# Performance work log

Hardware: AMD Instinct MI355X
Metric: run time of the kernel (lower is better)

Reference implementation:

```python
import jax, jax.numpy as jnp
import numpy as np

N_NODES = 50000


def _gcn_norm(edge_index, num_nodes):
    # PyG GCNConv default: add self-loops, symmetric normalization D^-1/2 A D^-1/2
    src, dst = edge_index[0], edge_index[1]
    loops = jnp.arange(num_nodes, dtype=src.dtype)
    src = jnp.concatenate([src, loops])
    dst = jnp.concatenate([dst, loops])
    deg = jax.ops.segment_sum(jnp.ones_like(src, dtype=jnp.float32), dst,
                              num_segments=num_nodes)
    dis = jnp.where(deg > 0, jax.lax.rsqrt(jnp.maximum(deg, 1.0)), 0.0)
    norm = dis[src] * dis[dst]  # [E']
    return src, dst, norm


def _gcn_conv(x, W, b, src, dst, norm, num_nodes):
    h = x @ W                                   # [N, out] transform first
    msg = h[src] * norm[:, None]                # [E', out] gather + scale
    agg = jax.ops.segment_sum(msg, dst, num_segments=num_nodes)  # scatter-add
    return agg + b


def setup_inputs() -> dict:
    key = jax.random.key(0)
    k1, k2, k3, k4 = jax.random.split(key, 4)
    n, e, d_in, d_h = N_NODES, 800000, 256, 128
    basic_block = jax.random.normal(k1, (n, d_in), dtype=jnp.float32)
    edge_index = jax.random.randint(k2, (2, e), 0, n, dtype=jnp.int64)
    W1 = jax.random.normal(k3, (d_in, d_h), dtype=jnp.float32) * (1.0 / np.sqrt(d_in))
    b1 = jnp.zeros((d_h,), dtype=jnp.float32)
    W2 = jax.random.normal(k4, (d_h, d_h), dtype=jnp.float32) * (1.0 / np.sqrt(d_h))
    b2 = jnp.zeros((d_h,), dtype=jnp.float32)
    return {"basic_block": basic_block, "edge_index": edge_index,
            "W1": W1, "b1": b1, "W2": W2, "b2": b2}


def reference(basic_block, edge_index, W1, b1, W2, b2):
    n = basic_block.shape[0]
    src, dst, norm = _gcn_norm(edge_index, n)
    x = jax.nn.relu(_gcn_conv(basic_block, W1, b1, src, dst, norm, n))
    x = _gcn_conv(x, W2, b2, src, dst, norm, n)
    return x
```

## Files before the change

### kernel.cpp

```cpp
#include <hip/hip_runtime.h>
#include <hip/hip_bf16.h>
#include <stdint.h>

#define D_H 128

typedef __bf16 bf16_t;
typedef unsigned short u16;
typedef bf16_t bf16x8 __attribute__((ext_vector_type(8)));
typedef bf16_t bf16x4 __attribute__((ext_vector_type(4)));
typedef float  f32x4  __attribute__((ext_vector_type(4)));

__global__ void k_countrank(const int* __restrict__ dst, int* __restrict__ cnt,
                            u16* __restrict__ rank, int E, int crBlocks,
                            const float* __restrict__ W1, bf16_t* __restrict__ W1h,
                            bf16_t* __restrict__ W1l, int K1,
                            const float* __restrict__ W2, bf16_t* __restrict__ W2h,
                            bf16_t* __restrict__ W2l, int K2) {
    if ((int)blockIdx.x < crBlocks) {
        int e = blockIdx.x * 256 + threadIdx.x;
        if (e < E) rank[e] = (u16)atomicAdd(&cnt[dst[e]], 1);
        return;
    }
    int id = ((int)blockIdx.x - crBlocks) * 256 + threadIdx.x;
    int n1 = K1 * 128;
    if (id < n1) {
        int k = id >> 7, n = id & 127;
        float w = W1[id];
        bf16_t h = (bf16_t)w;
        W1h[(size_t)n * K1 + k] = h;
        W1l[(size_t)n * K1 + k] = (bf16_t)(w - (float)h);
    } else if (id < n1 + K2 * 128) {
        int id2 = id - n1;
        int k = id2 >> 7, n = id2 & 127;
        float w = W2[id2];
        bf16_t h = (bf16_t)w;
        W2h[(size_t)n * K2 + k] = h;
        W2l[(size_t)n * K2 + k] = (bf16_t)(w - (float)h);
    }
}

__global__ __launch_bounds__(1024) void k_scan1(const int* __restrict__ cnt,
                                                int* __restrict__ out,
                                                int* __restrict__ bsums,
                                                float* __restrict__ dis, int N) {
    __shared__ int tmp[1024];
    int t = threadIdx.x;
    int i = blockIdx.x * 1024 + t;
    int v = (i < N) ? cnt[i] : 0;
    if (i < N) dis[i] = 1.0f / sqrtf((float)(v + 1));
    tmp[t] = v;
    __syncthreads();
    for (int d = 1; d < 1024; d <<= 1) {
        int x = (t >= d) ? tmp[t - d] : 0;
        __syncthreads();
        tmp[t] += x;
        __syncthreads();
    }
    if (i < N) out[i] = tmp[t] - v;
    if (t == 1023) bsums[blockIdx.x] = tmp[t];
}

__global__ void k_scan2(int* __restrict__ bsums, int nb) {
    __shared__ int tmp[64];
    int t = threadIdx.x;
    int v = (t < nb) ? bsums[t] : 0;
    tmp[t] = v;
    __syncthreads();
    for (int d = 1; d < 64; d <<= 1) {
        int x = (t >= d) ? tmp[t - d] : 0;
        __syncthreads();
        tmp[t] += x;
        __syncthreads();
    }
    if (t < nb) bsums[t] = tmp[t] - v;
}

__global__ __launch_bounds__(1024) void k_scan3(int* __restrict__ off,
                                                const int* __restrict__ bsums,
                                                int N, int E) {
    int i = blockIdx.x * 1024 + threadIdx.x;
    if (i < N) off[i] += bsums[blockIdx.x];
    if (i == 0) off[N] = E;
}

#define LDK 40
#define FILL_PER 8
__global__ __launch_bounds__(128) void k_mm1fill(
        const float* __restrict__ Af,
        const bf16_t* __restrict__ Wh, const bf16_t* __restrict__ Wl,
        const float* __restrict__ dis, bf16_t* __restrict__ Cb,
        int N, int K,
        const int* __restrict__ src, const int* __restrict__ dst,
        const int* __restrict__ off, const u16* __restrict__ rank,
        u16* __restrict__ csr16, int E, int totThreads) {
    __shared__ bf16_t AsH[64][LDK];
    __shared__ bf16_t AsL[64][LDK];
    __shared__ bf16_t BsH[128][LDK];
    __shared__ bf16_t BsL[128][LDK];

    const int t    = threadIdx.x;
    const int lane = t & 63;
    const int wave = t >> 6;
    const int row0 = blockIdx.x * 64;
    const int wn   = wave * 64;
    const int fm   = lane & 15;
    const int fq   = lane >> 4;

    const int g = blockIdx.x * 128 + t;
    int epos[FILL_PER];
    u16 esrc[FILL_PER];
#pragma unroll
    for (int i = 0; i < FILL_PER; i++) {
        int e = g + i * totThreads;
        if (e < E) {
            int d = dst[e];
            epos[i] = off[d] + (int)rank[e];
            esrc[i] = (u16)src[e];
        } else {
            epos[i] = -1;
            esrc[i] = 0;
        }
    }

    f32x4 acc[4][4] = {};

    for (int k0 = 0; k0 < K; k0 += 32) {
        __syncthreads();
#pragma unroll
        for (int i = 0; i < 4; i++) {
            int idx = t + i * 128;
            int r   = idx >> 3;
            int c4  = idx & 7;
            int gr  = row0 + r;
            float4 v = make_float4(0.f, 0.f, 0.f, 0.f);
            if (gr < N) v = *(const float4*)(Af + (size_t)gr * K + k0 + c4 * 4);
            bf16_t h0 = (bf16_t)v.x, h1 = (bf16_t)v.y, h2 = (bf16_t)v.z, h3 = (bf16_t)v.w;
            bf16_t l0 = (bf16_t)(v.x - (float)h0);
            bf16_t l1 = (bf16_t)(v.y - (float)h1);
            bf16_t l2 = (bf16_t)(v.z - (float)h2);
            bf16_t l3 = (bf16_t)(v.w - (float)h3);
            *(bf16x4*)&AsH[r][c4 * 4] = (bf16x4){h0, h1, h2, h3};
            *(bf16x4*)&AsL[r][c4 * 4] = (bf16x4){l0, l1, l2, l3};
        }
#pragma unroll
        for (int i = 0; i < 4; i++) {
            int idx = t + i * 128;
            int r   = idx >> 2;
            int c8  = idx & 3;
            *(bf16x8*)&BsH[r][c8 * 8] = *(const bf16x8*)(Wh + (size_t)r * K + k0 + c8 * 8);
            *(bf16x8*)&BsL[r][c8 * 8] = *(const bf16x8*)(Wl + (size_t)r * K + k0 + c8 * 8);
        }
        __syncthreads();

        bf16x8 ah[4], al[4], bh[4], bl[4];
#pragma unroll
        for (int i = 0; i < 4; i++) {
            ah[i] = *(const bf16x8*)&AsH[i * 16 + fm][fq * 8];
            al[i] = *(const bf16x8*)&AsL[i * 16 + fm][fq * 8];
            bh[i] = *(const bf16x8*)&BsH[wn + i * 16 + fm][fq * 8];
            bl[i] = *(const bf16x8*)&BsL[wn + i * 16 + fm][fq * 8];
        }
#pragma unroll
        for (int mi = 0; mi < 4; mi++)
#pragma unroll
            for (int ni = 0; ni < 4; ni++) {
                acc[mi][ni] = __builtin_amdgcn_mfma_f32_16x16x32_bf16(ah[mi], bh[ni], acc[mi][ni], 0, 0, 0);
                acc[mi][ni] = __builtin_amdgcn_mfma_f32_16x16x32_bf16(ah[mi], bl[ni], acc[mi][ni], 0, 0, 0);
                acc[mi][ni] = __builtin_amdgcn_mfma_f32_16x16x32_bf16(al[mi], bh[ni], acc[mi][ni], 0, 0, 0);
            }
    }

#pragma unroll
    for (int mi = 0; mi < 4; mi++)
#pragma unroll
        for (int r = 0; r < 4; r++) {
            int grow = row0 + mi * 16 + fq * 4 + r;
            if (grow < N) {
                float dr = dis[grow];
#pragma unroll
                for (int ni = 0; ni < 4; ni++)
                    Cb[(size_t)grow * D_H + wn + ni * 16 + fm] = (bf16_t)(dr * acc[mi][ni][r]);
            }
        }

#pragma unroll
    for (int i = 0; i < FILL_PER; i++)
        if (epos[i] >= 0) csr16[epos[i]] = esrc[i];
}

__global__ __launch_bounds__(128) void k_mm2(const bf16_t* __restrict__ Ah,
                                             const bf16_t* __restrict__ Al,
                                             const bf16_t* __restrict__ Wh,
                                             const bf16_t* __restrict__ Wl,
                                             const float* __restrict__ dis,
                                             bf16_t* __restrict__ Cb,
                                             int N, int K) {
    __shared__ bf16_t AsH[64][LDK];
    __shared__ bf16_t AsL[64][LDK];
    __shared__ bf16_t BsH[128][LDK];
    __shared__ bf16_t BsL[128][LDK];

    const int t    = threadIdx.x;
    const int lane = t & 63;
    const int wave = t >> 6;
    const int row0 = blockIdx.x * 64;
    const int wn   = wave * 64;
    const int fm   = lane & 15;
    const int fq   = lane >> 4;

    f32x4 acc[4][4] = {};

    for (int k0 = 0; k0 < K; k0 += 32) {
        __syncthreads();
#pragma unroll
        for (int i = 0; i < 2; i++) {
            int idx = t + i * 128;
            int r   = idx >> 2;
            int c8  = idx & 3;
            int gr  = row0 + r;
            bf16x8 vh = {}, vl = {};
            if (gr < N) {
                vh = *(const bf16x8*)(Ah + (size_t)gr * K + k0 + c8 * 8);
                vl = *(const bf16x8*)(Al + (size_t)gr * K + k0 + c8 * 8);
            }
            *(bf16x8*)&AsH[r][c8 * 8] = vh;
            *(bf16x8*)&AsL[r][c8 * 8] = vl;
        }
#pragma unroll
        for (int i = 0; i < 4; i++) {
            int idx = t + i * 128;
            int r   = idx >> 2;
            int c8  = idx & 3;
            *(bf16x8*)&BsH[r][c8 * 8] = *(const bf16x8*)(Wh + (size_t)r * K + k0 + c8 * 8);
            *(bf16x8*)&BsL[r][c8 * 8] = *(const bf16x8*)(Wl + (size_t)r * K + k0 + c8 * 8);
        }
        __syncthreads();

        bf16x8 ah[4], al[4], bh[4], bl[4];
#pragma unroll
        for (int i = 0; i < 4; i++) {
            ah[i] = *(const bf16x8*)&AsH[i * 16 + fm][fq * 8];
            al[i] = *(const bf16x8*)&AsL[i * 16 + fm][fq * 8];
            bh[i] = *(const bf16x8*)&BsH[wn + i * 16 + fm][fq * 8];
            bl[i] = *(const bf16x8*)&BsL[wn + i * 16 + fm][fq * 8];
        }
#pragma unroll
        for (int mi = 0; mi < 4; mi++)
#pragma unroll
            for (int ni = 0; ni < 4; ni++) {
                acc[mi][ni] = __builtin_amdgcn_mfma_f32_16x16x32_bf16(ah[mi], bh[ni], acc[mi][ni], 0, 0, 0);
                acc[mi][ni] = __builtin_amdgcn_mfma_f32_16x16x32_bf16(ah[mi], bl[ni], acc[mi][ni], 0, 0, 0);
                acc[mi][ni] = __builtin_amdgcn_mfma_f32_16x16x32_bf16(al[mi], bh[ni], acc[mi][ni], 0, 0, 0);
            }
    }

#pragma unroll
    for (int mi = 0; mi < 4; mi++)
#pragma unroll
        for (int r = 0; r < 4; r++) {
            int grow = row0 + mi * 16 + fq * 4 + r;
            if (grow < N) {
                float dr = dis[grow];
#pragma unroll
                for (int ni = 0; ni < 4; ni++)
                    Cb[(size_t)grow * D_H + wn + ni * 16 + fm] = (bf16_t)(dr * acc[mi][ni][r]);
            }
        }
}

__global__ __launch_bounds__(256) void k_agg(const bf16_t* __restrict__ Hb,
                                             const float* __restrict__ dis,
                                             const int* __restrict__ off,
                                             const u16* __restrict__ csr16,
                                             const float4* __restrict__ bias4,
                                             float4* __restrict__ outF,
                                             bf16_t* __restrict__ outH,
                                             bf16_t* __restrict__ outL,
                                             int N, int mode) {
    const int half = threadIdx.x >> 5;
    const int lane = threadIdx.x & 31;
    const int node = blockIdx.x * 8 + half;
    if (node >= N) return;

    const size_t loff = (size_t)lane * 4;

    bf16x4 vs = *(const bf16x4*)(Hb + (size_t)node * D_H + loff);
    float4 a0 = make_float4((float)vs[0], (float)vs[1], (float)vs[2], (float)vs[3]);
    float4 a1 = {0,0,0,0}, a2 = {0,0,0,0}, a3 = {0,0,0,0};
    float4 a4 = {0,0,0,0}, a5 = {0,0,0,0}, a6 = {0,0,0,0}, a7 = {0,0,0,0};

    int p  = off[node];
    int p1 = off[node + 1];

    for (; p + 8 <= p1; p += 8) {
        int s0 = (int)csr16[p + 0], s1 = (int)csr16[p + 1];
        int s2 = (int)csr16[p + 2], s3 = (int)csr16[p + 3];
        int s4 = (int)csr16[p + 4], s5 = (int)csr16[p + 5];
        int s6 = (int)csr16[p + 6], s7 = (int)csr16[p + 7];
        bf16x4 h0 = *(const bf16x4*)(Hb + (size_t)s0 * D_H + loff);
        bf16x4 h1 = *(const bf16x4*)(Hb + (size_t)s1 * D_H + loff);
        bf16x4 h2 = *(const bf16x4*)(Hb + (size_t)s2 * D_H + loff);
        bf16x4 h3 = *(const bf16x4*)(Hb + (size_t)s3 * D_H + loff);
        bf16x4 h4 = *(const bf16x4*)(Hb + (size_t)s4 * D_H + loff);
        bf16x4 h5 = *(const bf16x4*)(Hb + (size_t)s5 * D_H + loff);
        bf16x4 h6 = *(const bf16x4*)(Hb + (size_t)s6 * D_H + loff);
        bf16x4 h7 = *(const bf16x4*)(Hb + (size_t)s7 * D_H + loff);
        a0.x += (float)h0[0]; a0.y += (float)h0[1]; a0.z += (float)h0[2]; a0.w += (float)h0[3];
        a1.x += (float)h1[0]; a1.y += (float)h1[1]; a1.z += (float)h1[2]; a1.w += (float)h1[3];
        a2.x += (float)h2[0]; a2.y += (float)h2[1]; a2.z += (float)h2[2]; a2.w += (float)h2[3];
        a3.x += (float)h3[0]; a3.y += (float)h3[1]; a3.z += (float)h3[2]; a3.w += (float)h3[3];
        a4.x += (float)h4[0]; a4.y += (float)h4[1]; a4.z += (float)h4[2]; a4.w += (float)h4[3];
        a5.x += (float)h5[0]; a5.y += (float)h5[1]; a5.z += (float)h5[2]; a5.w += (float)h5[3];
        a6.x += (float)h6[0]; a6.y += (float)h6[1]; a6.z += (float)h6[2]; a6.w += (float)h6[3];
        a7.x += (float)h7[0]; a7.y += (float)h7[1]; a7.z += (float)h7[2]; a7.w += (float)h7[3];
    }
    if (p + 4 <= p1) {
        int s0 = (int)csr16[p + 0], s1 = (int)csr16[p + 1];
        int s2 = (int)csr16[p + 2], s3 = (int)csr16[p + 3];
        bf16x4 h0 = *(const bf16x4*)(Hb + (size_t)s0 * D_H + loff);
        bf16x4 h1 = *(const bf16x4*)(Hb + (size_t)s1 * D_H + loff);
        bf16x4 h2 = *(const bf16x4*)(Hb + (size_t)s2 * D_H + loff);
        bf16x4 h3 = *(const bf16x4*)(Hb + (size_t)s3 * D_H + loff);
        a0.x += (float)h0[0]; a0.y += (float)h0[1]; a0.z += (float)h0[2]; a0.w += (float)h0[3];
        a1.x += (float)h1[0]; a1.y += (float)h1[1]; a1.z += (float)h1[2]; a1.w += (float)h1[3];
        a2.x += (float)h2[0]; a2.y += (float)h2[1]; a2.z += (float)h2[2]; a2.w += (float)h2[3];
        a3.x += (float)h3[0]; a3.y += (float)h3[1]; a3.z += (float)h3[2]; a3.w += (float)h3[3];
        p += 4;
    }
    for (; p < p1; p++) {
        int s0 = (int)csr16[p];
        bf16x4 h0 = *(const bf16x4*)(Hb + (size_t)s0 * D_H + loff);
        a0.x += (float)h0[0]; a0.y += (float)h0[1]; a0.z += (float)h0[2]; a0.w += (float)h0[3];
    }

    float4 sum;
    sum.x = ((a0.x + a1.x) + (a2.x + a3.x)) + ((a4.x + a5.x) + (a6.x + a7.x));
    sum.y = ((a0.y + a1.y) + (a2.y + a3.y)) + ((a4.y + a5.y) + (a6.y + a7.y));
    sum.z = ((a0.z + a1.z) + (a2.z + a3.z)) + ((a4.z + a5.z) + (a6.z + a7.z));
    sum.w = ((a0.w + a1.w) + (a2.w + a3.w)) + ((a4.w + a5.w) + (a6.w + a7.w));

    const float  di = dis[node];
    const float4 bv = bias4[lane];
    float vx = fmaf(di, sum.x, bv.x);
    float vy = fmaf(di, sum.y, bv.y);
    float vz = fmaf(di, sum.z, bv.z);
    float vw = fmaf(di, sum.w, bv.w);

    if (mode == 1) {
        vx = fmaxf(vx, 0.0f); vy = fmaxf(vy, 0.0f);
        vz = fmaxf(vz, 0.0f); vw = fmaxf(vw, 0.0f);
        bf16_t hx = (bf16_t)vx, hy = (bf16_t)vy, hz = (bf16_t)vz, hw = (bf16_t)vw;
        bf16_t lx = (bf16_t)(vx - (float)hx);
        bf16_t ly = (bf16_t)(vy - (float)hy);
        bf16_t lz = (bf16_t)(vz - (float)hz);
        bf16_t lw = (bf16_t)(vw - (float)hw);
        *(bf16x4*)(outH + (size_t)node * D_H + loff) = (bf16x4){hx, hy, hz, hw};
        *(bf16x4*)(outL + (size_t)node * D_H + loff) = (bf16x4){lx, ly, lz, lw};
    } else {
        outF[(size_t)node * 32 + lane] = make_float4(vx, vy, vz, vw);
    }
}

extern "C" void kernel_launch(void* const* d_in, const int* in_sizes, int n_in,
                              void* d_out, int out_size, void* d_ws, size_t ws_size,
                              hipStream_t stream) {
    const float* X  = (const float*)d_in[0];
    const int*   ei = (const int*)d_in[1];
    const float* W1 = (const float*)d_in[2];
    const float* b1 = (const float*)d_in[3];
    const float* W2 = (const float*)d_in[4];
    const float* b2 = (const float*)d_in[5];
    float* out = (float*)d_out;

    const int N  = in_sizes[0] / 256;
    const int E  = in_sizes[1] / 2;
    const int K1 = 256;

    const int* src = ei;
    const int* dst = ei + E;

    uintptr_t p = (uintptr_t)d_ws;
    auto carve = [&](size_t bytes) {
        uintptr_t q = p;
        p += (bytes + 255) & ~(size_t)255;
        return q;
    };
    int*    cnt   = (int*)carve((size_t)N * 4);
    int*    off   = (int*)carve((size_t)(N + 1) * 4);
    int*    bsums = (int*)carve(64 * 4);
    float*  dis   = (float*)carve((size_t)N * 4);
    u16*    rank  = (u16*)carve((size_t)E * 2);
    u16*    csr16 = (u16*)carve((size_t)E * 2);
    bf16_t* Hb    = (bf16_t*)carve((size_t)N * D_H * 2);
    bf16_t* X1h   = (bf16_t*)carve((size_t)N * D_H * 2);
    bf16_t* X1l   = (bf16_t*)carve((size_t)N * D_H * 2);
    bf16_t* W1h   = (bf16_t*)carve((size_t)K1 * D_H * 2);
    bf16_t* W1l   = (bf16_t*)carve((size_t)K1 * D_H * 2);
    bf16_t* W2h   = (bf16_t*)carve((size_t)D_H * D_H * 2);
    bf16_t* W2l   = (bf16_t*)carve((size_t)D_H * D_H * 2);

    const int nb = (N + 1023) / 1024;

    hipMemsetAsync(cnt, 0, (size_t)N * 4, stream);
    const int gcr   = (E + 255) / 256;
    const int gprep = (K1 * 128 + D_H * 128 + 255) / 256;
    k_countrank<<<gcr + gprep, 256, 0, stream>>>(dst, cnt, rank, E, gcr,
                                                 W1, W1h, W1l, K1,
                                                 W2, W2h, W2l, D_H);
    k_scan1<<<nb, 1024, 0, stream>>>(cnt, off, bsums, dis, N);
    k_scan2<<<1, 64, 0, stream>>>(bsums, nb);
    k_scan3<<<nb, 1024, 0, stream>>>(off, bsums, N, E);

    const int gmm = (N + 63) / 64;
    const int gag = (N + 7) / 8;

    k_mm1fill<<<gmm, 128, 0, stream>>>(X, W1h, W1l, dis, Hb, N, K1,
                                       src, dst, off, rank, csr16, E, gmm * 128);
    k_agg<<<gag, 256, 0, stream>>>(Hb, dis, off, csr16,
                                   (const float4*)b1, nullptr, X1h, X1l, N, 1);

    k_mm2<<<gmm, 128, 0, stream>>>(X1h, X1l, W2h, W2l, dis, Hb, N, D_H);
    k_agg<<<gag, 256, 0, stream>>>(Hb, dis, off, csr16,
                                   (const float4*)b2, (float4*)out, nullptr, nullptr, N, 0);
}
```

Before: 265.4 us.

## Split GEMM output columns across blocks and use four waves per block

Both GEMM kernels now compute a 64x64 output tile per block instead of 64x128. Launches use 256 threads (4 waves in a 2x2 layout of 32x32 sub-tiles), and the grid doubles. The goal is more parallelism and occupancy: each wave holds fewer accumulators, so more blocks can be resident. The cost is that every block re-reads and re-converts the A rows (fp32 to hi/lo bf16 in mm1), so A traffic and conversion work double. The CSR fill spread is reduced to 2 edges per thread to match the larger thread count.

```diff
diff --git a/kernel.cpp b/kernel.cpp
--- a/kernel.cpp
+++ b/kernel.cpp
@@ -84,8 +84,9 @@
 }
 
 #define LDK 40
-#define FILL_PER 8
-__global__ __launch_bounds__(128) void k_mm1fill(
+#define FILL_PER 2
+
+__global__ __launch_bounds__(256) void k_mm1fill(
         const float* __restrict__ Af,
         const bf16_t* __restrict__ Wh, const bf16_t* __restrict__ Wl,
         const float* __restrict__ dis, bf16_t* __restrict__ Cb,
@@ -95,18 +96,20 @@
         u16* __restrict__ csr16, int E, int totThreads) {
     __shared__ bf16_t AsH[64][LDK];
     __shared__ bf16_t AsL[64][LDK];
-    __shared__ bf16_t BsH[128][LDK];
-    __shared__ bf16_t BsL[128][LDK];
+    __shared__ bf16_t BsH[64][LDK];
+    __shared__ bf16_t BsL[64][LDK];
 
     const int t    = threadIdx.x;
     const int lane = t & 63;
     const int wave = t >> 6;
-    const int row0 = blockIdx.x * 64;
-    const int wn   = wave * 64;
+    const int row0 = ((int)blockIdx.x >> 1) * 64;
+    const int col0 = ((int)blockIdx.x & 1) * 64;
+    const int wm   = (wave & 1) * 32;
+    const int wn   = (wave >> 1) * 32;
     const int fm   = lane & 15;
     const int fq   = lane >> 4;
 
-    const int g = blockIdx.x * 128 + t;
+    const int g = (int)blockIdx.x * 256 + t;
     int epos[FILL_PER];
     u16 esrc[FILL_PER];
 #pragma unroll
@@ -122,13 +125,13 @@
         }
     }
 
-    f32x4 acc[4][4] = {};
+    f32x4 acc[2][2] = {};
 
     for (int k0 = 0; k0 < K; k0 += 32) {
         __syncthreads();
 #pragma unroll
-        for (int i = 0; i < 4; i++) {
-            int idx = t + i * 128;
+        for (int i = 0; i < 2; i++) {
+            int idx = t + i * 256;
             int r   = idx >> 3;
             int c4  = idx & 7;
             int gr  = row0 + r;
@@ -142,28 +145,26 @@
             *(bf16x4*)&AsH[r][c4 * 4] = (bf16x4){h0, h1, h2, h3};
             *(bf16x4*)&AsL[r][c4 * 4] = (bf16x4){l0, l1, l2, l3};
         }
-#pragma unroll
-        for (int i = 0; i < 4; i++) {
-            int idx = t + i * 128;
-            int r   = idx >> 2;
-            int c8  = idx & 3;
-            *(bf16x8*)&BsH[r][c8 * 8] = *(const bf16x8*)(Wh + (size_t)r * K + k0 + c8 * 8);
-            *(bf16x8*)&BsL[r][c8 * 8] = *(const bf16x8*)(Wl + (size_t)r * K + k0 + c8 * 8);
-        }
-        __syncthreads();
-
-        bf16x8 ah[4], al[4], bh[4], bl[4];
-#pragma unroll
-        for (int i = 0; i < 4; i++) {
-            ah[i] = *(const bf16x8*)&AsH[i * 16 + fm][fq * 8];
-            al[i] = *(const bf16x8*)&AsL[i * 16 + fm][fq * 8];
+        {
+            int r  = t >> 2;
+            int c8 = t & 3;
+            *(bf16x8*)&BsH[r][c8 * 8] = *(const bf16x8*)(Wh + (size_t)(col0 + r) * K + k0 + c8 * 8);
+            *(bf16x8*)&BsL[r][c8 * 8] = *(const bf16x8*)(Wl + (size_t)(col0 + r) * K + k0 + c8 * 8);
+        }
+        __syncthreads();
+
+        bf16x8 ah[2], al[2], bh[2], bl[2];
+#pragma unroll
+        for (int i = 0; i < 2; i++) {
+            ah[i] = *(const bf16x8*)&AsH[wm + i * 16 + fm][fq * 8];
+            al[i] = *(const bf16x8*)&AsL[wm + i * 16 + fm][fq * 8];
             bh[i] = *(const bf16x8*)&BsH[wn + i * 16 + fm][fq * 8];
             bl[i] = *(const bf16x8*)&BsL[wn + i * 16 + fm][fq * 8];
         }
 #pragma unroll
-        for (int mi = 0; mi < 4; mi++)
-#pragma unroll
-            for (int ni = 0; ni < 4; ni++) {
+        for (int mi = 0; mi < 2; mi++)
+#pragma unroll
+            for (int ni = 0; ni < 2; ni++) {
                 acc[mi][ni] = __builtin_amdgcn_mfma_f32_16x16x32_bf16(ah[mi], bh[ni], acc[mi][ni], 0, 0, 0);
                 acc[mi][ni] = __builtin_amdgcn_mfma_f32_16x16x32_bf16(ah[mi], bl[ni], acc[mi][ni], 0, 0, 0);
                 acc[mi][ni] = __builtin_amdgcn_mfma_f32_16x16x32_bf16(al[mi], bh[ni], acc[mi][ni], 0, 0, 0);
@@ -171,15 +172,15 @@
     }
 
 #pragma unroll
-    for (int mi = 0; mi < 4; mi++)
+    for (int mi = 0; mi < 2; mi++)
 #pragma unroll
         for (int r = 0; r < 4; r++) {
-            int grow = row0 + mi * 16 + fq * 4 + r;
+            int grow = row0 + wm + mi * 16 + fq * 4 + r;
             if (grow < N) {
                 float dr = dis[grow];
 #pragma unroll
-                for (int ni = 0; ni < 4; ni++)
-                    Cb[(size_t)grow * D_H + wn + ni * 16 + fm] = (bf16_t)(dr * acc[mi][ni][r]);
+                for (int ni = 0; ni < 2; ni++)
+                    Cb[(size_t)grow * D_H + col0 + wn + ni * 16 + fm] = (bf16_t)(dr * acc[mi][ni][r]);
             }
         }
 
@@ -188,7 +189,7 @@
         if (epos[i] >= 0) csr16[epos[i]] = esrc[i];
 }
 
-__global__ __launch_bounds__(128) void k_mm2(const bf16_t* __restrict__ Ah,
+__global__ __launch_bounds__(256) void k_mm2(const bf16_t* __restrict__ Ah,
                                              const bf16_t* __restrict__ Al,
                                              const bf16_t* __restrict__ Wh,
                                              const bf16_t* __restrict__ Wl,
@@ -197,27 +198,27 @@
                                              int N, int K) {
     __shared__ bf16_t AsH[64][LDK];
     __shared__ bf16_t AsL[64][LDK];
-    __shared__ bf16_t BsH[128][LDK];
-    __shared__ bf16_t BsL[128][LDK];
+    __shared__ bf16_t BsH[64][LDK];
+    __shared__ bf16_t BsL[64][LDK];
 
     const int t    = threadIdx.x;
     const int lane = t & 63;
     const int wave = t >> 6;
-    const int row0 = blockIdx.x * 64;
-    const int wn   = wave * 64;
+    const int row0 = ((int)blockIdx.x >> 1) * 64;
+    const int col0 = ((int)blockIdx.x & 1) * 64;
+    const int wm   = (wave & 1) * 32;
+    const int wn   = (wave >> 1) * 32;
     const int fm   = lane & 15;
     const int fq   = lane >> 4;
 
-    f32x4 acc[4][4] = {};
+    f32x4 acc[2][2] = {};
 
     for (int k0 = 0; k0 < K; k0 += 32) {
         __syncthreads();
-#pragma unroll
-        for (int i = 0; i < 2; i++) {
-            int idx = t + i * 128;
-            int r   = idx >> 2;
-            int c8  = idx & 3;
-            int gr  = row0 + r;
+        {
+            int r  = t >> 2;
+            int c8 = t & 3;
+            int gr = row0 + r;
             bf16x8 vh = {}, vl = {};
             if (gr < N) {
                 vh = *(const bf16x8*)(Ah + (size_t)gr * K + k0 + c8 * 8);
@@ -226,28 +227,26 @@
             *(bf16x8*)&AsH[r][c8 * 8] = vh;
             *(bf16x8*)&AsL[r][c8 * 8] = vl;
         }
-#pragma unroll
-        for (int i = 0; i < 4; i++) {
-            int idx = t + i * 128;
-            int r   = idx >> 2;
-            int c8  = idx & 3;
-            *(bf16x8*)&BsH[r][c8 * 8] = *(const bf16x8*)(Wh + (size_t)r * K + k0 + c8 * 8);
-            *(bf16x8*)&BsL[r][c8 * 8] = *(const bf16x8*)(Wl + (size_t)r * K + k0 + c8 * 8);
-        }
-        __syncthreads();
-
-        bf16x8 ah[4], al[4], bh[4], bl[4];
-#pragma unroll
-        for (int i = 0; i < 4; i++) {
-            ah[i] = *(const bf16x8*)&AsH[i * 16 + fm][fq * 8];
-            al[i] = *(const bf16x8*)&AsL[i * 16 + fm][fq * 8];
+        {
+            int r  = t >> 2;
+            int c8 = t & 3;
+            *(bf16x8*)&BsH[r][c8 * 8] = *(const bf16x8*)(Wh + (size_t)(col0 + r) * K + k0 + c8 * 8);
+            *(bf16x8*)&BsL[r][c8 * 8] = *(const bf16x8*)(Wl + (size_t)(col0 + r) * K + k0 + c8 * 8);
+        }
+        __syncthreads();
+
+        bf16x8 ah[2], al[2], bh[2], bl[2];
+#pragma unroll
+        for (int i = 0; i < 2; i++) {
+            ah[i] = *(const bf16x8*)&AsH[wm + i * 16 + fm][fq * 8];
+            al[i] = *(const bf16x8*)&AsL[wm + i * 16 + fm][fq * 8];
             bh[i] = *(const bf16x8*)&BsH[wn + i * 16 + fm][fq * 8];
             bl[i] = *(const bf16x8*)&BsL[wn + i * 16 + fm][fq * 8];
         }
 #pragma unroll
-        for (int mi = 0; mi < 4; mi++)
-#pragma unroll
-            for (int ni = 0; ni < 4; ni++) {
+        for (int mi = 0; mi < 2; mi++)
+#pragma unroll
+            for (int ni = 0; ni < 2; ni++) {
                 acc[mi][ni] = __builtin_amdgcn_mfma_f32_16x16x32_bf16(ah[mi], bh[ni], acc[mi][ni], 0, 0, 0);
                 acc[mi][ni] = __builtin_amdgcn_mfma_f32_16x16x32_bf16(ah[mi], bl[ni], acc[mi][ni], 0, 0, 0);
                 acc[mi][ni] = __builtin_amdgcn_mfma_f32_16x16x32_bf16(al[mi], bh[ni], acc[mi][ni], 0, 0, 0);
@@ -255,15 +254,15 @@
     }
 
 #pragma unroll
-    for (int mi = 0; mi < 4; mi++)
+    for (int mi = 0; mi < 2; mi++)
 #pragma unroll
         for (int r = 0; r < 4; r++) {
-            int grow = row0 + mi * 16 + fq * 4 + r;
+            int grow = row0 + wm + mi * 16 + fq * 4 + r;
             if (grow < N) {
                 float dr = dis[grow];
 #pragma unroll
-                for (int ni = 0; ni < 4; ni++)
-                    Cb[(size_t)grow * D_H + wn + ni * 16 + fm] = (bf16_t)(dr * acc[mi][ni][r]);
+                for (int ni = 0; ni < 2; ni++)
+                    Cb[(size_t)grow * D_H + col0 + wn + ni * 16 + fm] = (bf16_t)(dr * acc[mi][ni][r]);
             }
         }
 }
@@ -411,15 +410,15 @@
     k_scan2<<<1, 64, 0, stream>>>(bsums, nb);
     k_scan3<<<nb, 1024, 0, stream>>>(off, bsums, N, E);
 
-    const int gmm = (N + 63) / 64;
+    const int gmm = ((N + 63) / 64) * 2;
     const int gag = (N + 7) / 8;
 
-    k_mm1fill<<<gmm, 128, 0, stream>>>(X, W1h, W1l, dis, Hb, N, K1,
-                                       src, dst, off, rank, csr16, E, gmm * 128);
+    k_mm1fill<<<gmm, 256, 0, stream>>>(X, W1h, W1l, dis, Hb, N, K1,
+                                       src, dst, off, rank, csr16, E, gmm * 256);
     k_agg<<<gag, 256, 0, stream>>>(Hb, dis, off, csr16,
                                    (const float4*)b1, nullptr, X1h, X1l, N, 1);
 
-    k_mm2<<<gmm, 128, 0, stream>>>(X1h, X1l, W2h, W2l, dis, Hb, N, D_H);
+    k_mm2<<<gmm, 256, 0, stream>>>(X1h, X1l, W2h, W2l, dis, Hb, N, D_H);
     k_agg<<<gag, 256, 0, stream>>>(Hb, dis, off, csr16,
                                    (const float4*)b2, (float4*)out, nullptr, nullptr, N, 0);
 }
```

Result: faster. 251.4 us (-5.3%).
